# Kernel tuning notes

Hardware: AMD Instinct MI355X
Metric: run time of the kernel (lower is better)

Reference implementation:

```python
import jax, jax.numpy as jnp
import numpy as np

B, S, D, H = 2, 2048, 1024, 16
HD = D // H
SCALE = HD ** -0.5


def setup_inputs() -> dict:
    key = jax.random.key(0)
    ks = jax.random.split(key, 9)
    w = 0.02
    return {
        "query": jax.random.normal(ks[0], (B, S, D), jnp.float32),
        "key": jax.random.normal(ks[1], (B, S, D), jnp.float32),
        "value": jax.random.normal(ks[2], (B, S, D), jnp.float32),
        # precomputed structural bias matrix B_struct [B, S, S]
        "bias_struct": jax.random.uniform(ks[3], (B, S, S), jnp.float32, 0.0, 1.5),
        "Wq": jax.random.normal(ks[4], (D, D), jnp.float32) * w,
        "bq": jnp.zeros((D,), jnp.float32),
        "Wk": jax.random.normal(ks[5], (D, D), jnp.float32) * w,
        "bk": jnp.zeros((D,), jnp.float32),
        "Wv": jax.random.normal(ks[6], (D, D), jnp.float32) * w,
        "bv": jnp.zeros((D,), jnp.float32),
        "Wo": jax.random.normal(ks[7], (D, D), jnp.float32) * w,
        "bo": jnp.zeros((D,), jnp.float32),
        "lambda_bias": jnp.array(1.0, jnp.float32),
    }


def _split_heads(x):
    # [B, S, D] -> [B, H, S, HD]
    b, s, _ = x.shape
    return x.reshape(b, s, H, HD).transpose(0, 2, 1, 3)


def reference(query, key, value, bias_struct, Wq, bq, Wk, bk, Wv, bv, Wo, bo, lambda_bias):
    # Linear projections (torch Linear: x @ W.T + b)
    Q = _split_heads(query @ Wq.T + bq)
    K = _split_heads(key @ Wk.T + bk)
    V = _split_heads(value @ Wv.T + bv)
    # scores = QK^T * scale + lambda * B_struct (broadcast over heads)
    scores = jnp.einsum("bhqd,bhkd->bhqk", Q, K) * SCALE
    scores = scores + lambda_bias * bias_struct[:, None, :, :]
    attn = jax.nn.softmax(scores, axis=-1)
    out = jnp.einsum("bhqk,bhkd->bhqd", attn, V)
    out = out.transpose(0, 2, 1, 3).reshape(query.shape[0], query.shape[1], D)
    return out @ Wo.T + bo
```

## Files before the change

kernel.cpp:

```cpp
#include <hip/hip_runtime.h>
#include <hip/hip_bf16.h>

namespace {

constexpr int B  = 2;
constexpr int S  = 2048;
constexpr int D  = 1024;
constexpr int H  = 16;
constexpr int BH = B * H;
constexpr float SCALE = 0.125f;
constexpr float THR = 8.0f;

constexpr int GM = B * S;
constexpr int GN = D;
constexpr int GK = D;

typedef __bf16 bf16x8 __attribute__((ext_vector_type(8)));
typedef float  f32x4  __attribute__((ext_vector_type(4)));
typedef unsigned short u16;
typedef u16 u16x8 __attribute__((ext_vector_type(8)));
typedef u16 u16x4 __attribute__((ext_vector_type(4)));

__device__ __forceinline__ u16 f2bf(float f) {
  union { float f; unsigned u; } v{f};
  unsigned r = v.u + 0x7fffu + ((v.u >> 16) & 1u);
  return (u16)(r >> 16);
}
__device__ __forceinline__ float bf2f(u16 u) {
  union { unsigned u; float f; } v{(unsigned)u << 16};
  return v.f;
}

__device__ __forceinline__ f32x4 mfma16(bf16x8 a, bf16x8 b, f32x4 c) {
  return __builtin_amdgcn_mfma_f32_16x16x32_bf16(a, b, c, 0, 0, 0);
}

__device__ __forceinline__ void gload_lds16(const u16* g, u16* l) {
  __builtin_amdgcn_global_load_lds(
      (const __attribute__((address_space(1))) void*)g,
      (__attribute__((address_space(3))) void*)l, 16, 0, 0);
}

__global__ __launch_bounds__(256) void cvt3_k(
    const float* __restrict__ a, const float* __restrict__ b,
    const float* __restrict__ c, u16* __restrict__ da,
    u16* __restrict__ db, u16* __restrict__ dc)
{
  const float* s = (blockIdx.z == 0) ? a : (blockIdx.z == 1) ? b : c;
  u16* d = (blockIdx.z == 0) ? da : (blockIdx.z == 1) ? db : dc;
  size_t i = ((size_t)blockIdx.x * 256 + threadIdx.x) * 4;
  float4 v = *(const float4*)&s[i];
  u16x4 o = { f2bf(v.x), f2bf(v.y), f2bf(v.z), f2bf(v.w) };
  *(u16x4*)&d[i] = o;
}

__global__ __launch_bounds__(256) void cvt4_k(
    const float* __restrict__ a, const float* __restrict__ b,
    const float* __restrict__ c, const float* __restrict__ e,
    u16* __restrict__ da, u16* __restrict__ db,
    u16* __restrict__ dc, u16* __restrict__ de)
{
  const float* s = (blockIdx.z == 0) ? a : (blockIdx.z == 1) ? b
                 : (blockIdx.z == 2) ? c : e;
  u16* d = (blockIdx.z == 0) ? da : (blockIdx.z == 1) ? db
         : (blockIdx.z == 2) ? dc : de;
  size_t i = ((size_t)blockIdx.x * 256 + threadIdx.x) * 4;
  float4 v = *(const float4*)&s[i];
  u16x4 o = { f2bf(v.x), f2bf(v.y), f2bf(v.z), f2bf(v.w) };
  *(u16x4*)&d[i] = o;
}

template <bool OUTBF, int NZ>
__global__ __launch_bounds__(256) void gemm_k(
    const u16* __restrict__ A0, const u16* __restrict__ A1, const u16* __restrict__ A2,
    const u16* __restrict__ W0, const u16* __restrict__ W1, const u16* __restrict__ W2,
    const float* __restrict__ b0, const float* __restrict__ b1, const float* __restrict__ b2,
    u16* __restrict__ C0, u16* __restrict__ C1, u16* __restrict__ C2,
    float* __restrict__ Cf)
{
  constexpr int BM = 128, BN = 64, BK = 64;
  __shared__ u16 Al[2][BM * BK];
  __shared__ u16 Bl[2][BN * BK];

  const int z = (NZ > 1) ? blockIdx.z : 0;
  const u16* Ap = (z == 0) ? A0 : (z == 1) ? A1 : A2;
  const u16* Wp = (z == 0) ? W0 : (z == 1) ? W1 : W2;
  const float* bias = (z == 0) ? b0 : (z == 1) ? b1 : b2;
  u16* Cb = (z == 0) ? C0 : (z == 1) ? C1 : C2;

  const int tid  = threadIdx.x;
  const int lane = tid & 63;
  const int w    = tid >> 6;
  const int wr = w >> 1, wc = w & 1;
  const int lg = lane >> 4, ll = lane & 15;
  const int bm = blockIdx.y * BM, bn = blockIdx.x * BN;

  auto STAGE = [&](int buf, int k0) {
#pragma unroll
    for (int i = 0; i < 4; ++i) {
      const int c = i * 256 + tid;
      const int row = c >> 3, cs = c & 7;
      const int dofs = ((cs * 16) ^ ((row & 7) << 4)) >> 1;
      gload_lds16(&Ap[(size_t)(bm + row) * GK + k0 + dofs], &Al[buf][c * 8]);
    }
#pragma unroll
    for (int i = 0; i < 2; ++i) {
      const int c = i * 256 + tid;
      const int row = c >> 3, cs = c & 7;
      const int dofs = ((cs * 16) ^ ((row & 7) << 4)) >> 1;
      gload_lds16(&Wp[(size_t)(bn + row) * GK + k0 + dofs], &Bl[buf][c * 8]);
    }
  };

  f32x4 acc[4][2] = {};

  STAGE(0, 0);
  __syncthreads();

  int cur = 0;
  constexpr int NT = GK / BK;
  for (int t = 0; t < NT; ++t) {
    if (t + 1 < NT) STAGE(cur ^ 1, (t + 1) * BK);
#pragma unroll
    for (int half = 0; half < 2; ++half) {
      bf16x8 af[4], bfr[2];
#pragma unroll
      for (int mi = 0; mi < 4; ++mi) {
        const int row = wr * 64 + mi * 16 + ll;
        af[mi] = *(const bf16x8*)&Al[cur][row * 64 +
                   (((half * 64 + lg * 16) ^ ((row & 7) << 4)) >> 1)];
      }
#pragma unroll
      for (int ni = 0; ni < 2; ++ni) {
        const int row = wc * 32 + ni * 16 + ll;
        bfr[ni] = *(const bf16x8*)&Bl[cur][row * 64 +
                   (((half * 64 + lg * 16) ^ ((row & 7) << 4)) >> 1)];
      }
#pragma unroll
      for (int mi = 0; mi < 4; ++mi)
#pragma unroll
        for (int ni = 0; ni < 2; ++ni)
          acc[mi][ni] = mfma16(af[mi], bfr[ni], acc[mi][ni]);
    }
    __syncthreads();
    cur ^= 1;
  }

#pragma unroll
  for (int ni = 0; ni < 2; ++ni) {
    const int gcol = bn + wc * 32 + ni * 16 + ll;
    const float bv = bias[gcol];
#pragma unroll
    for (int mi = 0; mi < 4; ++mi) {
      const int grow = bm + wr * 64 + mi * 16 + lg * 4;
#pragma unroll
      for (int r = 0; r < 4; ++r) {
        float v = acc[mi][ni][r] + bv;
        if (OUTBF) Cb[(size_t)(grow + r) * GN + gcol] = f2bf(v);
        else       Cf[(size_t)(grow + r) * GN + gcol] = v;
      }
    }
  }
}

__global__ __launch_bounds__(256) void transpose_v_k(
    const u16* __restrict__ Vb, u16* __restrict__ Vt)
{
  __shared__ u16 T[64][72];
  const int tid = threadIdx.x;
  const int bh = blockIdx.y, b = bh >> 4, h = bh & 15;
  const int s0 = blockIdx.x * 64;
#pragma unroll
  for (int it = 0; it < 2; ++it) {
    int idx = tid + it * 256;
    int s = idx >> 3, dc = idx & 7;
    *(uint4*)&T[s][dc * 8] =
        *(const uint4*)&Vb[(size_t)(b * S + s0 + s) * D + h * 64 + dc * 8];
  }
  __syncthreads();
#pragma unroll
  for (int it = 0; it < 2; ++it) {
    int idx = tid + it * 256;
    int d = idx >> 3, sc = idx & 7;
    u16x8 o;
#pragma unroll
    for (int jj = 0; jj < 8; ++jj) o[jj] = T[sc * 8 + jj][d];
    *(u16x8*)&Vt[((size_t)bh * 64 + d) * S + s0 + sc * 8] = o;
  }
}

__global__ __launch_bounds__(256) void attn_split_k(
    const u16* __restrict__ Qb, const u16* __restrict__ Kb,
    const u16* __restrict__ Vt, const float* __restrict__ biasS,
    const float* __restrict__ lamp, u16* __restrict__ Opart,
    float2* __restrict__ Ml)
{
  __shared__ u16 Kl[2][64 * 64];
  __shared__ __bf16 Pl[4][16][72];

  const int tid  = threadIdx.x;
  const int lane = tid & 63;
  const int w    = tid >> 6;
  const int lg = lane >> 4, ll = lane & 15;
  const int bh = blockIdx.y, b = bh >> 4, h = bh & 15;
  const int qw = blockIdx.x * 64 + w * 16;
  const int split = blockIdx.z;
  const int kvbase = split * (S / 2);
  const float lam = lamp[0];

  bf16x8 aQ[2];
  {
    const u16* qrow = &Qb[(size_t)(b * S + qw + ll) * D + h * 64];
    aQ[0] = *(const bf16x8*)&qrow[lg * 8];
    aQ[1] = *(const bf16x8*)&qrow[32 + lg * 8];
  }

  const u16* Kbase = &Kb[(size_t)(b * S + kvbase) * D + h * 64];
  const u16* Vbase = &Vt[(size_t)bh * 64 * S + kvbase];
  const float* Bb  = &biasS[((size_t)b * S + qw + lg * 4) * S + kvbase];

  auto STAGE_K = [&](int buf, int k0) {
#pragma unroll
    for (int i = 0; i < 2; ++i) {
      const int c   = (w * 2 + i) * 64 + lane;
      const int row = c >> 3, cs = c & 7;
      const int dofs = ((cs * 16) ^ ((row & 7) << 4)) >> 1;
      gload_lds16(&Kbase[(size_t)(k0 + row) * D + dofs],
                  &Kl[buf][(w * 2 + i) * 512]);
    }
  };

  f32x4 accO[4] = {};
  float m_r[4], l_r[4];
#pragma unroll
  for (int r = 0; r < 4; ++r) { m_r[r] = -1e30f; l_r[r] = 0.f; }

  float bc[4][4];
  STAGE_K(0, 0);
#pragma unroll
  for (int r = 0; r < 4; ++r)
#pragma unroll
    for (int kf = 0; kf < 4; ++kf)
      bc[r][kf] = Bb[(size_t)r * S + kf * 16 + ll];
  __syncthreads();

  int cur = 0;
  constexpr int NT = (S / 2) / 64;
  for (int t = 0; t < NT; ++t) {
    const int k0 = t * 64;
    if (t + 1 < NT) STAGE_K(cur ^ 1, k0 + 64);

    bf16x8 v0[4], v1[4];
#pragma unroll
    for (int nf = 0; nf < 4; ++nf) {
      const u16* vrow = &Vbase[(size_t)(nf * 16 + ll) * S + k0];
      v0[nf] = *(const bf16x8*)&vrow[lg * 8];
      v1[nf] = *(const bf16x8*)&vrow[32 + lg * 8];
    }
    float bnx[4][4];
    if (t + 1 < NT) {
#pragma unroll
      for (int r = 0; r < 4; ++r)
#pragma unroll
        for (int kf = 0; kf < 4; ++kf)
          bnx[r][kf] = Bb[(size_t)r * S + k0 + 64 + kf * 16 + ll];
    }

    f32x4 sf[4];
#pragma unroll
    for (int kf = 0; kf < 4; ++kf) {
      const int row = kf * 16 + ll;
      const u16* kr = &Kl[cur][row * 64];
      bf16x8 kb0 = *(const bf16x8*)&kr[((lg * 16) ^ ((row & 7) << 4)) >> 1];
      bf16x8 kb1 = *(const bf16x8*)&kr[((64 + lg * 16) ^ ((row & 7) << 4)) >> 1];
      f32x4 t4 = {0.f, 0.f, 0.f, 0.f};
      t4 = mfma16(aQ[0], kb0, t4);
      t4 = mfma16(aQ[1], kb1, t4);
#pragma unroll
      for (int r = 0; r < 4; ++r)
        t4[r] = t4[r] * SCALE + lam * bc[r][kf];
      sf[kf] = t4;
    }

    float pm[4];
#pragma unroll
    for (int r = 0; r < 4; ++r)
      pm[r] = fmaxf(fmaxf(sf[0][r], sf[1][r]), fmaxf(sf[2][r], sf[3][r]));
    float ex = fmaxf(fmaxf(pm[0] - m_r[0], pm[1] - m_r[1]),
                     fmaxf(pm[2] - m_r[2], pm[3] - m_r[3]));
    if (__any(ex > THR)) {
#pragma unroll
      for (int r = 0; r < 4; ++r) {
        float tmx = pm[r];
        tmx = fmaxf(tmx, __shfl_xor(tmx, 1));
        tmx = fmaxf(tmx, __shfl_xor(tmx, 2));
        tmx = fmaxf(tmx, __shfl_xor(tmx, 4));
        tmx = fmaxf(tmx, __shfl_xor(tmx, 8));
        float nm = fmaxf(m_r[r], tmx);
        float cf = __expf(m_r[r] - nm);
        m_r[r] = nm;
        l_r[r] *= cf;
#pragma unroll
        for (int nf = 0; nf < 4; ++nf) accO[nf][r] *= cf;
      }
    }
#pragma unroll
    for (int r = 0; r < 4; ++r) {
      float ps = 0.f;
#pragma unroll
      for (int kf = 0; kf < 4; ++kf) {
        float p = __expf(sf[kf][r] - m_r[r]);
        Pl[w][lg * 4 + r][kf * 16 + ll] = (__bf16)p;
        ps += p;
      }
      l_r[r] += ps;
    }

    bf16x8 aP0 = *(const bf16x8*)&Pl[w][ll][lg * 8];
    bf16x8 aP1 = *(const bf16x8*)&Pl[w][ll][32 + lg * 8];
#pragma unroll
    for (int nf = 0; nf < 4; ++nf) {
      accO[nf] = mfma16(aP0, v0[nf], accO[nf]);
      accO[nf] = mfma16(aP1, v1[nf], accO[nf]);
    }

    if (t + 1 < NT) {
#pragma unroll
      for (int r = 0; r < 4; ++r)
#pragma unroll
        for (int kf = 0; kf < 4; ++kf) bc[r][kf] = bnx[r][kf];
    }
    __syncthreads();
    cur ^= 1;
  }

#pragma unroll
  for (int r = 0; r < 4; ++r) {
    float tl = l_r[r];
    tl += __shfl_xor(tl, 1);
    tl += __shfl_xor(tl, 2);
    tl += __shfl_xor(tl, 4);
    tl += __shfl_xor(tl, 8);
    l_r[r] = tl;
  }

  u16* Op = Opart + (size_t)split * ((size_t)BH * S * 64);
  float2* Mlp = Ml + (size_t)split * ((size_t)BH * S);
  if (ll == 0) {
#pragma unroll
    for (int r = 0; r < 4; ++r) {
      float2 v; v.x = m_r[r]; v.y = l_r[r];
      Mlp[(size_t)bh * S + qw + lg * 4 + r] = v;
    }
  }
#pragma unroll
  for (int nf = 0; nf < 4; ++nf)
#pragma unroll
    for (int r = 0; r < 4; ++r)
      Op[((size_t)bh * S + qw + lg * 4 + r) * 64 + nf * 16 + ll] =
          f2bf(accO[nf][r]);
}

__global__ __launch_bounds__(256) void merge_k(
    const u16* __restrict__ Opart, const float2* __restrict__ Ml,
    u16* __restrict__ Obf)
{
  const int tid = threadIdx.x;
  const size_t row = (size_t)blockIdx.x * 32 + (tid >> 3);
  const int dc = (tid & 7) * 8;
  const float2 ml0 = Ml[row];
  const float2 ml1 = Ml[(size_t)BH * S + row];
  const float m = fmaxf(ml0.x, ml1.x);
  float c0 = __expf(ml0.x - m), c1 = __expf(ml1.x - m);
  const float inv = 1.0f / (c0 * ml0.y + c1 * ml1.y);
  c0 *= inv; c1 *= inv;
  u16x8 a = *(const u16x8*)&Opart[row * 64 + dc];
  u16x8 bq = *(const u16x8*)&Opart[(size_t)BH * S * 64 + row * 64 + dc];
  u16x8 o;
#pragma unroll
  for (int j = 0; j < 8; ++j)
    o[j] = f2bf(c0 * bf2f(a[j]) + c1 * bf2f(bq[j]));
  const int bh = (int)(row >> 11), q = (int)(row & 2047);
  *(u16x8*)&Obf[((size_t)((bh >> 4) * S + q)) * D + (bh & 15) * 64 + dc] = o;
}

}

extern "C" void kernel_launch(void* const* d_in, const int* in_sizes, int n_in,
                              void* d_out, int out_size, void* d_ws, size_t ws_size,
                              hipStream_t stream)
{
  const float* query = (const float*)d_in[0];
  const float* key   = (const float*)d_in[1];
  const float* value = (const float*)d_in[2];
  const float* biasS = (const float*)d_in[3];
  const float* Wq = (const float*)d_in[4];
  const float* bq = (const float*)d_in[5];
  const float* Wk = (const float*)d_in[6];
  const float* bk = (const float*)d_in[7];
  const float* Wv = (const float*)d_in[8];
  const float* bv = (const float*)d_in[9];
  const float* Wo = (const float*)d_in[10];
  const float* bo = (const float*)d_in[11];
  const float* lam = (const float*)d_in[12];
  float* out = (float*)d_out;

  char* ws = (char*)d_ws;
  const size_t MB = 1024 * 1024;
  u16* Xq  = (u16*)(ws + 0 * MB);
  u16* Xk  = (u16*)(ws + 8 * MB);
  u16* Xv  = (u16*)(ws + 16 * MB);
  u16* WqB = (u16*)(ws + 24 * MB);
  u16* WkB = (u16*)(ws + 26 * MB);
  u16* WvB = (u16*)(ws + 28 * MB);
  u16* WoB = (u16*)(ws + 30 * MB);
  u16* Qbf = (u16*)(ws + 32 * MB);
  u16* Kbf = (u16*)(ws + 40 * MB);
  u16* Opart = (u16*)ws;
  u16* Obf   = (u16*)(ws + 16 * MB);
  u16* Vbf = (u16*)d_out;
  u16* Vt  = (u16*)d_out + (size_t)4 * MB;
  float2* Ml = (float2*)d_out;

  cvt3_k<<<dim3(4096, 1, 3), 256, 0, stream>>>(query, key, value, Xq, Xk, Xv);
  cvt4_k<<<dim3(1024, 1, 4), 256, 0, stream>>>(Wq, Wk, Wv, Wo, WqB, WkB, WvB, WoB);

  dim3 pgrid(GN / 64, GM / 128, 3);
  gemm_k<true, 3><<<pgrid, 256, 0, stream>>>(
      Xq, Xk, Xv, WqB, WkB, WvB, bq, bk, bv, Qbf, Kbf, Vbf, nullptr);

  transpose_v_k<<<dim3(S / 64, B * H), 256, 0, stream>>>(Vbf, Vt);

  attn_split_k<<<dim3(S / 64, BH, 2), 256, 0, stream>>>(
      Qbf, Kbf, Vt, biasS, lam, Opart, Ml);

  merge_k<<<dim3(BH * S / 32), 256, 0, stream>>>(Opart, Ml, Obf);

  dim3 ogrid(GN / 64, GM / 128, 1);
  gemm_k<false, 1><<<ogrid, 256, 0, stream>>>(
      Obf, nullptr, nullptr, WoB, nullptr, nullptr, bo, nullptr, nullptr,
      nullptr, nullptr, nullptr, out);
}
```

Baseline: 405.3 us.

## Fold bias into MFMA accumulator, use exp2 domain, drop register prefetch of V and bias

The attention kernel now seeds the QK^T MFMA accumulator with lambda*8*bias and applies a single scale*log2e multiply afterwards, so softmax runs in base 2 with exp2f. The rescale threshold and the merge kernel are converted to the same domain. The software prefetch of the next tile's bias and the early V loads into registers are removed; both are now loaded just before use. This cuts register pressure and ALU work, but exposes global-load latency for bias and V inside the loop.

```diff
diff --git a/kernel.cpp b/kernel.cpp
--- a/kernel.cpp
+++ b/kernel.cpp
@@ -9,7 +9,9 @@
 constexpr int H  = 16;
 constexpr int BH = B * H;
 constexpr float SCALE = 0.125f;
-constexpr float THR = 8.0f;
+constexpr float LOG2E = 1.44269504f;
+constexpr float SL2   = SCALE * LOG2E;
+constexpr float THR2  = 8.0f * LOG2E;
 
 constexpr int GM = B * S;
 constexpr int GN = D;
@@ -206,7 +208,7 @@
   const int qw = blockIdx.x * 64 + w * 16;
   const int split = blockIdx.z;
   const int kvbase = split * (S / 2);
-  const float lam = lamp[0];
+  const float lamS = lamp[0] * 8.0f;
 
   bf16x8 aQ[2];
   {
@@ -235,13 +237,7 @@
 #pragma unroll
   for (int r = 0; r < 4; ++r) { m_r[r] = -1e30f; l_r[r] = 0.f; }
 
-  float bc[4][4];
   STAGE_K(0, 0);
-#pragma unroll
-  for (int r = 0; r < 4; ++r)
-#pragma unroll
-    for (int kf = 0; kf < 4; ++kf)
-      bc[r][kf] = Bb[(size_t)r * S + kf * 16 + ll];
   __syncthreads();
 
   int cur = 0;
@@ -250,22 +246,6 @@
     const int k0 = t * 64;
     if (t + 1 < NT) STAGE_K(cur ^ 1, k0 + 64);
 
-    bf16x8 v0[4], v1[4];
-#pragma unroll
-    for (int nf = 0; nf < 4; ++nf) {
-      const u16* vrow = &Vbase[(size_t)(nf * 16 + ll) * S + k0];
-      v0[nf] = *(const bf16x8*)&vrow[lg * 8];
-      v1[nf] = *(const bf16x8*)&vrow[32 + lg * 8];
-    }
-    float bnx[4][4];
-    if (t + 1 < NT) {
-#pragma unroll
-      for (int r = 0; r < 4; ++r)
-#pragma unroll
-        for (int kf = 0; kf < 4; ++kf)
-          bnx[r][kf] = Bb[(size_t)r * S + k0 + 64 + kf * 16 + ll];
-    }
-
     f32x4 sf[4];
 #pragma unroll
     for (int kf = 0; kf < 4; ++kf) {
@@ -273,12 +253,14 @@
       const u16* kr = &Kl[cur][row * 64];
       bf16x8 kb0 = *(const bf16x8*)&kr[((lg * 16) ^ ((row & 7) << 4)) >> 1];
       bf16x8 kb1 = *(const bf16x8*)&kr[((64 + lg * 16) ^ ((row & 7) << 4)) >> 1];
-      f32x4 t4 = {0.f, 0.f, 0.f, 0.f};
+      f32x4 t4;
+#pragma unroll
+      for (int r = 0; r < 4; ++r)
+        t4[r] = lamS * Bb[(size_t)r * S + k0 + kf * 16 + ll];
       t4 = mfma16(aQ[0], kb0, t4);
       t4 = mfma16(aQ[1], kb1, t4);
 #pragma unroll
-      for (int r = 0; r < 4; ++r)
-        t4[r] = t4[r] * SCALE + lam * bc[r][kf];
+      for (int r = 0; r < 4; ++r) t4[r] *= SL2;
       sf[kf] = t4;
     }
 
@@ -288,7 +270,7 @@
       pm[r] = fmaxf(fmaxf(sf[0][r], sf[1][r]), fmaxf(sf[2][r], sf[3][r]));
     float ex = fmaxf(fmaxf(pm[0] - m_r[0], pm[1] - m_r[1]),
                      fmaxf(pm[2] - m_r[2], pm[3] - m_r[3]));
-    if (__any(ex > THR)) {
+    if (__any(ex > THR2)) {
 #pragma unroll
       for (int r = 0; r < 4; ++r) {
         float tmx = pm[r];
@@ -297,7 +279,7 @@
         tmx = fmaxf(tmx, __shfl_xor(tmx, 4));
         tmx = fmaxf(tmx, __shfl_xor(tmx, 8));
         float nm = fmaxf(m_r[r], tmx);
-        float cf = __expf(m_r[r] - nm);
+        float cf = exp2f(m_r[r] - nm);
         m_r[r] = nm;
         l_r[r] *= cf;
 #pragma unroll
@@ -309,7 +291,7 @@
       float ps = 0.f;
 #pragma unroll
       for (int kf = 0; kf < 4; ++kf) {
-        float p = __expf(sf[kf][r] - m_r[r]);
+        float p = exp2f(sf[kf][r] - m_r[r]);
         Pl[w][lg * 4 + r][kf * 16 + ll] = (__bf16)p;
         ps += p;
       }
@@ -320,16 +302,13 @@
     bf16x8 aP1 = *(const bf16x8*)&Pl[w][ll][32 + lg * 8];
 #pragma unroll
     for (int nf = 0; nf < 4; ++nf) {
-      accO[nf] = mfma16(aP0, v0[nf], accO[nf]);
-      accO[nf] = mfma16(aP1, v1[nf], accO[nf]);
-    }
-
-    if (t + 1 < NT) {
-#pragma unroll
-      for (int r = 0; r < 4; ++r)
-#pragma unroll
-        for (int kf = 0; kf < 4; ++kf) bc[r][kf] = bnx[r][kf];
-    }
+      const u16* vrow = &Vbase[(size_t)(nf * 16 + ll) * S + k0];
+      bf16x8 v0 = *(const bf16x8*)&vrow[lg * 8];
+      bf16x8 v1 = *(const bf16x8*)&vrow[32 + lg * 8];
+      accO[nf] = mfma16(aP0, v0, accO[nf]);
+      accO[nf] = mfma16(aP1, v1, accO[nf]);
+    }
+
     __syncthreads();
     cur ^= 1;
   }
@@ -371,7 +350,7 @@
   const float2 ml0 = Ml[row];
   const float2 ml1 = Ml[(size_t)BH * S + row];
   const float m = fmaxf(ml0.x, ml1.x);
-  float c0 = __expf(ml0.x - m), c1 = __expf(ml1.x - m);
+  float c0 = exp2f(ml0.x - m), c1 = exp2f(ml1.x - m);
   const float inv = 1.0f / (c0 * ml0.y + c1 * ml1.y);
   c0 *= inv; c1 *= inv;
   u16x8 a = *(const u16x8*)&Opart[row * 64 + dc];
```

Measured after the change: 387.6 us. 1.05x faster.
